# Performance work log

Measured on AMD Instinct MI355X. Metric: run time of the kernel, lower is better.

Reference implementation:

```python
import jax, jax.numpy as jnp
import numpy as np

B, S, DM, H = 2, 2048, 1024, 16
HD = DM // H


def setup_inputs() -> dict:
    key = jax.random.key(0)
    ks = jax.random.split(key, 12)
    xavier = lambda k: jax.random.uniform(k, (DM, DM), jnp.float32,
                                          -np.sqrt(6.0 / (DM + DM)), np.sqrt(6.0 / (DM + DM)))
    return {
        "q": jax.random.normal(ks[0], (B, S, DM), jnp.float32),
        "k": jax.random.normal(ks[1], (B, S, DM), jnp.float32),
        "v": jax.random.normal(ks[2], (B, S, DM), jnp.float32),
        "mask": jnp.ones((B, S, S), jnp.int32),
        "Wq": xavier(ks[3]), "bq": jnp.zeros((DM,), jnp.float32),
        "Wk": xavier(ks[4]), "bk": jnp.zeros((DM,), jnp.float32),
        "Wv": xavier(ks[5]), "bv": jnp.zeros((DM,), jnp.float32),
        "Wf": xavier(ks[6]), "bf": jnp.zeros((DM,), jnp.float32),
    }


def reference(q, k, v, mask, Wq, bq, Wk, bk, Wv, bv, Wf, bf):
    b, s, dm = q.shape
    # projections (torch Linear: x @ W.T + b)
    qh = (q @ Wq.T + bq).reshape(b, s, H, HD).transpose(0, 2, 1, 3)  # [B,H,S,HD]
    kh = (k @ Wk.T + bk).reshape(b, -1, H, HD).transpose(0, 2, 1, 3)
    vh = (v @ Wv.T + bv).reshape(b, -1, H, HD).transpose(0, 2, 1, 3)
    scores = jnp.einsum('bhqd,bhkd->bhqk', qh, kh) / np.sqrt(HD)    # [B,H,S,S]
    scores = jnp.where(mask[:, None, :, :] == 0, -jnp.inf, scores)
    attn = jax.nn.softmax(scores, axis=-1)
    out = jnp.einsum('bhqk,bhkd->bhqd', attn, vh)                   # [B,H,S,HD]
    out = out.transpose(0, 2, 1, 3).reshape(b, s, dm)
    return out @ Wf.T + bf, attn
```

## Files before the change

### kernel.cpp

```cpp
#include <hip/hip_runtime.h>
#include <stdint.h>


typedef _Float16 f16x8 __attribute__((ext_vector_type(8)));
typedef float f32x4 __attribute__((ext_vector_type(4)));
typedef unsigned long long ull;

static_assert(sizeof(f16x8) == 16, "f16x8 must be 16B");

#define MFMA16(a, b, c) __builtin_amdgcn_mfma_f32_16x16x32_f16((a), (b), (c), 0, 0, 0)

__device__ __forceinline__ unsigned short f2h_(float f) {
  _Float16 h = (_Float16)f;
  return __builtin_bit_cast(unsigned short, h);
}

__global__ __launch_bounds__(256) void cvt_kernel(
    const float* __restrict__ q, const float* __restrict__ k,
    const float* __restrict__ v, const float* __restrict__ wq,
    const float* __restrict__ wk, const float* __restrict__ wv,
    const float* __restrict__ wf, unsigned short* __restrict__ dst) {
  long e0 = ((long)blockIdx.x * 256 + threadIdx.x) * 8;
  const float* src; long off;
  if (e0 < 4194304L)       { src = q;  off = e0; }
  else if (e0 < 8388608L)  { src = k;  off = e0 - 4194304L; }
  else if (e0 < 12582912L) { src = v;  off = e0 - 8388608L; }
  else if (e0 < 13631488L) { src = wq; off = e0 - 12582912L; }
  else if (e0 < 14680064L) { src = wk; off = e0 - 13631488L; }
  else if (e0 < 15728640L) { src = wv; off = e0 - 14680064L; }
  else                     { src = wf; off = e0 - 15728640L; }
  float4 a = *(const float4*)(src + off);
  float4 b = *(const float4*)(src + off + 4);
  uint4 o;
  o.x = (unsigned)f2h_(a.x) | ((unsigned)f2h_(a.y) << 16);
  o.y = (unsigned)f2h_(a.z) | ((unsigned)f2h_(a.w) << 16);
  o.z = (unsigned)f2h_(b.x) | ((unsigned)f2h_(b.y) << 16);
  o.w = (unsigned)f2h_(b.z) | ((unsigned)f2h_(b.w) << 16);
  *(uint4*)(dst + e0) = o;
}

__global__ __launch_bounds__(256) void mask_pack(const int* __restrict__ mask,
                                                 ull* __restrict__ mb) {
  int wid = (int)((blockIdx.x * 256 + threadIdx.x) >> 6);
  int lane = threadIdx.x & 63;
  int nw = (int)((gridDim.x * 256) >> 6);
  for (int w = wid; w < 131072; w += nw) {
    int val = mask[(long)w * 64 + lane];
    ull bits = __ballot(val != 0);
    if (lane == 0) mb[w] = bits;
  }
}

__device__ __forceinline__ void gemm_body(
    const unsigned short* __restrict__ A, const unsigned short* __restrict__ Bm,
    const float* __restrict__ bias, unsigned short* __restrict__ outb,
    float* __restrict__ outf, int mode) {
  __shared__ unsigned short Al[128 * 64];
  __shared__ unsigned short Bl[128 * 64];
  const int tid = threadIdx.x, lane = tid & 63, wave = tid >> 6;
  const int lo = lane & 15, hi = lane >> 4;
  const int wi = wave >> 1, wj = wave & 1;
  const int ib = blockIdx.y << 7, jb = blockIdx.x << 7;
  const int cb0 = hi << 4;
  f32x4 acc[4][4] = {};
  for (int kt = 0; kt < 16; ++kt) {
    const int k0 = kt << 6;
    __syncthreads();
#pragma unroll
    for (int i = 0; i < 4; ++i) {
      int u = tid + (i << 8), r = u >> 3, c = u & 7;
      uint4 av = *(const uint4*)(A + (long)(ib + r) * 1024 + k0 + c * 8);
      uint4 bv = *(const uint4*)(Bm + (long)(jb + r) * 1024 + k0 + c * 8);
      *(uint4*)((char*)Al + r * 128 + ((c * 16) ^ ((r & 7) << 4))) = av;
      *(uint4*)((char*)Bl + r * 128 + ((c * 16) ^ ((r & 7) << 4))) = bv;
    }
    __syncthreads();
    f16x8 af[4][2], bfr[4][2];
#pragma unroll
    for (int it = 0; it < 4; ++it) {
      int r = (wi << 6) + (it << 4) + lo;
      af[it][0] = *(const f16x8*)((char*)Al + r * 128 + (cb0 ^ ((r & 7) << 4)));
      af[it][1] = *(const f16x8*)((char*)Al + r * 128 + ((64 + cb0) ^ ((r & 7) << 4)));
    }
#pragma unroll
    for (int jt = 0; jt < 4; ++jt) {
      int r = (wj << 6) + (jt << 4) + lo;
      bfr[jt][0] = *(const f16x8*)((char*)Bl + r * 128 + (cb0 ^ ((r & 7) << 4)));
      bfr[jt][1] = *(const f16x8*)((char*)Bl + r * 128 + ((64 + cb0) ^ ((r & 7) << 4)));
    }
#pragma unroll
    for (int it = 0; it < 4; ++it)
#pragma unroll
      for (int jt = 0; jt < 4; ++jt) {
        acc[it][jt] = MFMA16(af[it][0], bfr[jt][0], acc[it][jt]);
        acc[it][jt] = MFMA16(af[it][1], bfr[jt][1], acc[it][jt]);
      }
  }
#pragma unroll
  for (int it = 0; it < 4; ++it)
#pragma unroll
    for (int jt = 0; jt < 4; ++jt) {
      f32x4 vv = acc[it][jt];
      int i0 = ib + (wi << 6) + (it << 4) + (hi << 2);
      int j = jb + (wj << 6) + (jt << 4) + lo;
      float4 bb = *(const float4*)(bias + i0);
      vv[0] += bb.x; vv[1] += bb.y; vv[2] += bb.z; vv[3] += bb.w;
      if (mode == 2) {
        float4 st; st.x = vv[0]; st.y = vv[1]; st.z = vv[2]; st.w = vv[3];
        *(float4*)(outf + (long)j * 1024 + i0) = st;
      } else {
        int h = i0 >> 6, dd = i0 & 63, b2 = j >> 11, s2 = j & 2047;
        if (mode == 0) {
          ull pk = (ull)f2h_(vv[0]) | ((ull)f2h_(vv[1]) << 16) |
                   ((ull)f2h_(vv[2]) << 32) | ((ull)f2h_(vv[3]) << 48);
          *(ull*)(outb + ((long)((b2 * 16 + h) * 2048 + s2)) * 64 + dd) = pk;
        } else {
          unsigned short* p = outb + ((long)((b2 * 16 + h) * 64 + dd)) * 2048 + s2;
          p[0] = f2h_(vv[0]); p[2048] = f2h_(vv[1]);
          p[4096] = f2h_(vv[2]); p[6144] = f2h_(vv[3]);
        }
      }
    }
}

__global__ __launch_bounds__(256) void gemm_qkv(
    const unsigned short* __restrict__ xb, const float* __restrict__ bq,
    const float* __restrict__ bk, const float* __restrict__ bv,
    unsigned short* __restrict__ outbase) {
  const int z = blockIdx.z;
  const unsigned short* A = xb + 12582912 + (long)z * 1048576;
  const unsigned short* Bm = xb + (long)z * 4194304;
  const float* bias = (z == 0) ? bq : ((z == 1) ? bk : bv);
  unsigned short* outp = outbase + (long)z * 4194304;
  gemm_body(A, Bm, bias, outp, nullptr, (z == 2) ? 1 : 0);
}

__global__ __launch_bounds__(256) void gemm_f(
    const unsigned short* __restrict__ xb, const unsigned short* __restrict__ oh,
    const float* __restrict__ bias, float* __restrict__ outf) {
  gemm_body(xb + 15728640, oh, bias, nullptr, outf, 2);
}

__global__ __launch_bounds__(256) void attn_kernel(
    const unsigned short* __restrict__ qh, const unsigned short* __restrict__ kh,
    const unsigned short* __restrict__ vt, const ull* __restrict__ mb,
    float* __restrict__ attnp, unsigned short* __restrict__ oh) {
  __shared__ unsigned short Qs[64 * 64];
  __shared__ unsigned short Ks[128 * 64];
  __shared__ unsigned short Vs[64 * 128];
  __shared__ unsigned short Ps[64 * 128];
  const int tid = threadIdx.x, lane = tid & 63, wave = tid >> 6;
  const int lo = lane & 15, hi = lane >> 4;
  const int cb0 = hi << 4;
  int id = blockIdx.y * 32 + blockIdx.x;
  int wgid = (id & 7) * 128 + (id >> 3);
  const int bh = wgid >> 5, b_ = bh >> 4;
  const int q0 = (wgid & 31) << 6;
  const float cs = 0.18033688011112042f;

  {
    const unsigned short* qb = qh + ((long)bh * 2048 + q0) * 64;
#pragma unroll
    for (int i = 0; i < 2; ++i) {
      int u = tid + (i << 8), r = u >> 3, c = u & 7;
      uint4 d = *(const uint4*)(qb + r * 64 + c * 8);
      *(uint4*)((char*)Qs + r * 128 + ((c * 16) ^ ((r & 7) << 4))) = d;
    }
  }
  __syncthreads();
  const int rq = (wave << 4) + lo;
  const int qg = q0 + rq;
  const int swq = (rq & 7) << 4;
  f16x8 aq0 = *(const f16x8*)((char*)Qs + rq * 128 + (cb0 ^ swq));
  f16x8 aq1 = *(const f16x8*)((char*)Qs + rq * 128 + ((64 + cb0) ^ swq));
  const ull* mrow = mb + (long)(b_ * 2048 + qg) * 32;

  float ll = 0.f;
  f32x4 oacc[4] = {};

  for (int kt = 0; kt < 16; ++kt) {
    __syncthreads();
#pragma unroll
    for (int i = 0; i < 4; ++i) {
      int u = tid + (i << 8);
      { int r = u >> 3, c = u & 7;
        uint4 d = *(const uint4*)(kh + ((long)bh * 2048 + (kt << 7) + r) * 64 + c * 8);
        *(uint4*)((char*)Ks + r * 128 + ((c * 16) ^ ((r & 7) << 4))) = d; }
      { int r = u >> 4, c = u & 15;
        uint4 d = *(const uint4*)(vt + ((long)bh * 64 + r) * 2048 + (kt << 7) + c * 8);
        *(uint4*)((char*)Vs + r * 256 + ((c * 16) ^ ((r & 7) << 4))) = d; }
    }
    __syncthreads();
    f32x4 fa[8];
#pragma unroll
    for (int nt = 0; nt < 8; ++nt) {
      int rk = (nt << 4) + lo;
      int swk = (rk & 7) << 4;
      f16x8 k0 = *(const f16x8*)((char*)Ks + rk * 128 + (cb0 ^ swk));
      f16x8 k1 = *(const f16x8*)((char*)Ks + rk * 128 + ((64 + cb0) ^ swk));
      f32x4 z = {};
      z = MFMA16(k0, aq0, z);
      z = MFMA16(k1, aq1, z);
      fa[nt] = z;
    }
    ull mw0 = mrow[(kt << 1)], mw1 = mrow[(kt << 1) + 1];
    const bool fast = __all((mw0 & mw1) == ~0ull);
#pragma unroll
    for (int nt = 0; nt < 8; ++nt) {
      float e0 = __builtin_amdgcn_exp2f(fa[nt][0] * cs);
      float e1 = __builtin_amdgcn_exp2f(fa[nt][1] * cs);
      float e2 = __builtin_amdgcn_exp2f(fa[nt][2] * cs);
      float e3 = __builtin_amdgcn_exp2f(fa[nt][3] * cs);
      if (!fast) {
        int kb = (nt << 4) + (hi << 2);
        ull mws = (kb & 64) ? mw1 : mw0;
        int sh = kb & 63;
        if (!((mws >> sh) & 1ull)) e0 = 0.f;
        if (!((mws >> (sh + 1)) & 1ull)) e1 = 0.f;
        if (!((mws >> (sh + 2)) & 1ull)) e2 = 0.f;
        if (!((mws >> (sh + 3)) & 1ull)) e3 = 0.f;
      }
      ll += (e0 + e1) + (e2 + e3);
      ull pk = (ull)f2h_(e0) | ((ull)f2h_(e1) << 16) |
               ((ull)f2h_(e2) << 32) | ((ull)f2h_(e3) << 48);
      *(ull*)((char*)Ps + rq * 256 + (((nt << 5) + (hi << 3)) ^ swq)) = pk;
    }
    f16x8 ap[4];
#pragma unroll
    for (int ks = 0; ks < 4; ++ks)
      ap[ks] = *(const f16x8*)((char*)Ps + rq * 256 + (((ks << 6) + cb0) ^ swq));
#pragma unroll
    for (int nt = 0; nt < 4; ++nt) {
      int rv = (nt << 4) + lo;
      int swv = (rv & 7) << 4;
#pragma unroll
      for (int ks = 0; ks < 4; ++ks) {
        f16x8 bvv = *(const f16x8*)((char*)Vs + rv * 256 + (((ks << 6) + cb0) ^ swv));
        oacc[nt] = MFMA16(ap[ks], bvv, oacc[nt]);
      }
    }
  }
  ll += __shfl_xor(ll, 16);
  ll += __shfl_xor(ll, 32);
  const float rl = (ll > 0.f) ? (1.f / ll) : 0.f;

  float rlr[4];
#pragma unroll
  for (int r = 0; r < 4; ++r) rlr[r] = __shfl(rl, (hi << 2) + r, 16);
#pragma unroll
  for (int nt = 0; nt < 4; ++nt)
#pragma unroll
    for (int r = 0; r < 4; ++r) {
      int qe = q0 + (wave << 4) + (hi << 2) + r;
      oh[(long)(b_ * 2048 + qe) * 1024 + ((bh & 15) << 6) + (nt << 4) + lo] =
          f2h_(oacc[nt][r] * rlr[r]);
    }

  float* arow = attnp + ((long)bh * 2048 + qg) * 2048;
  for (int kt = 0; kt < 16; ++kt) {
    __syncthreads();
#pragma unroll
    for (int i = 0; i < 4; ++i) {
      int u = tid + (i << 8), r = u >> 3, c = u & 7;
      uint4 d = *(const uint4*)(kh + ((long)bh * 2048 + (kt << 7) + r) * 64 + c * 8);
      *(uint4*)((char*)Ks + r * 128 + ((c * 16) ^ ((r & 7) << 4))) = d;
    }
    __syncthreads();
    f32x4 fa[8];
#pragma unroll
    for (int nt = 0; nt < 8; ++nt) {
      int rk = (nt << 4) + lo;
      int swk = (rk & 7) << 4;
      f16x8 k0 = *(const f16x8*)((char*)Ks + rk * 128 + (cb0 ^ swk));
      f16x8 k1 = *(const f16x8*)((char*)Ks + rk * 128 + ((64 + cb0) ^ swk));
      f32x4 z = {};
      z = MFMA16(k0, aq0, z);
      z = MFMA16(k1, aq1, z);
      fa[nt] = z;
    }
    ull mw0 = mrow[(kt << 1)], mw1 = mrow[(kt << 1) + 1];
    const bool fast = __all((mw0 & mw1) == ~0ull);
#pragma unroll
    for (int nt = 0; nt < 8; ++nt) {
      float e0 = __builtin_amdgcn_exp2f(fa[nt][0] * cs) * rl;
      float e1 = __builtin_amdgcn_exp2f(fa[nt][1] * cs) * rl;
      float e2 = __builtin_amdgcn_exp2f(fa[nt][2] * cs) * rl;
      float e3 = __builtin_amdgcn_exp2f(fa[nt][3] * cs) * rl;
      if (!fast) {
        int kb = (nt << 4) + (hi << 2);
        ull mws = (kb & 64) ? mw1 : mw0;
        int sh = kb & 63;
        if (!((mws >> sh) & 1ull)) e0 = 0.f;
        if (!((mws >> (sh + 1)) & 1ull)) e1 = 0.f;
        if (!((mws >> (sh + 2)) & 1ull)) e2 = 0.f;
        if (!((mws >> (sh + 3)) & 1ull)) e3 = 0.f;
      }
      f32x4 st; st[0] = e0; st[1] = e1; st[2] = e2; st[3] = e3;
      __builtin_nontemporal_store(st, (f32x4*)(arow + (kt << 7) + (nt << 4) + (hi << 2)));
    }
  }
}

extern "C" void kernel_launch(void* const* d_in, const int* in_sizes, int n_in,
                              void* d_out, int out_size, void* d_ws, size_t ws_size,
                              hipStream_t stream) {
  const float* q = (const float*)d_in[0];
  const float* k = (const float*)d_in[1];
  const float* v = (const float*)d_in[2];
  const int* mask = (const int*)d_in[3];
  const float* Wq = (const float*)d_in[4];
  const float* bq = (const float*)d_in[5];
  const float* Wk = (const float*)d_in[6];
  const float* bk = (const float*)d_in[7];
  const float* Wv = (const float*)d_in[8];
  const float* bv = (const float*)d_in[9];
  const float* Wf = (const float*)d_in[10];
  const float* bf_ = (const float*)d_in[11];

  float* out = (float*)d_out;
  float* attn = out + 4194304;

  unsigned short* xb = (unsigned short*)d_ws;
  unsigned short* qhp = xb + 16777216;
  unsigned short* khp = qhp + 4194304;
  unsigned short* vtp = khp + 4194304;
  unsigned short* ohp = vtp + 4194304;
  ull* mb = (ull*)((char*)d_ws + 67108864);

  cvt_kernel<<<dim3(8192), dim3(256), 0, stream>>>(q, k, v, Wq, Wk, Wv, Wf, xb);
  mask_pack<<<dim3(512), dim3(256), 0, stream>>>(mask, mb);
  gemm_qkv<<<dim3(32, 8, 3), dim3(256), 0, stream>>>(xb, bq, bk, bv, qhp);
  attn_kernel<<<dim3(32, 32), dim3(256), 0, stream>>>(qhp, khp, vtp, mb, attn, ohp);
  gemm_f<<<dim3(32, 8), dim3(256), 0, stream>>>(xb, ohp, bf_, out);
}
```

Measured before the change: 315.1 us.

## Split attention into two kernels and load GEMM tiles directly into LDS

The GEMM tile loads now use global_load_lds so data goes straight into LDS, which drops the XOR swizzle and reads fragments from an unswizzled layout. The fused attention kernel is split in two. The first computes the output and the per-row reciprocal softmax sums, which go to workspace. The second recomputes the scores to write the normalized attention matrix and is launched after the final projection GEMM. Both attention kernels read K and V fragments straight from global memory instead of staging them in LDS, which removes the barriers. The trade-offs are possible LDS bank conflicts in the GEMM, less coalesced per-lane global fragment loads in attention, and an extra launch.

```diff
diff --git a/kernel.cpp b/kernel.cpp
--- a/kernel.cpp
+++ b/kernel.cpp
@@ -13,6 +13,12 @@
 __device__ __forceinline__ unsigned short f2h_(float f) {
   _Float16 h = (_Float16)f;
   return __builtin_bit_cast(unsigned short, h);
+}
+
+__device__ __forceinline__ void gload16(const void* g, void* l) {
+  __builtin_amdgcn_global_load_lds(
+      (const __attribute__((address_space(1))) unsigned int*)g,
+      (__attribute__((address_space(3))) unsigned int*)l, 16, 0, 0);
 }
 
 __global__ __launch_bounds__(256) void cvt_kernel(
@@ -62,31 +68,32 @@
   const int wi = wave >> 1, wj = wave & 1;
   const int ib = blockIdx.y << 7, jb = blockIdx.x << 7;
   const int cb0 = hi << 4;
+  const int sr = lane >> 3;
+  const int sc = (lane & 7) << 3;
   f32x4 acc[4][4] = {};
   for (int kt = 0; kt < 16; ++kt) {
     const int k0 = kt << 6;
     __syncthreads();
 #pragma unroll
     for (int i = 0; i < 4; ++i) {
-      int u = tid + (i << 8), r = u >> 3, c = u & 7;
-      uint4 av = *(const uint4*)(A + (long)(ib + r) * 1024 + k0 + c * 8);
-      uint4 bv = *(const uint4*)(Bm + (long)(jb + r) * 1024 + k0 + c * 8);
-      *(uint4*)((char*)Al + r * 128 + ((c * 16) ^ ((r & 7) << 4))) = av;
-      *(uint4*)((char*)Bl + r * 128 + ((c * 16) ^ ((r & 7) << 4))) = bv;
+      int ci = (i << 2) + wave;
+      int r = (ci << 3) + sr;
+      gload16(A + (long)(ib + r) * 1024 + k0 + sc, Al + (ci << 9));
+      gload16(Bm + (long)(jb + r) * 1024 + k0 + sc, Bl + (ci << 9));
     }
     __syncthreads();
     f16x8 af[4][2], bfr[4][2];
 #pragma unroll
     for (int it = 0; it < 4; ++it) {
       int r = (wi << 6) + (it << 4) + lo;
-      af[it][0] = *(const f16x8*)((char*)Al + r * 128 + (cb0 ^ ((r & 7) << 4)));
-      af[it][1] = *(const f16x8*)((char*)Al + r * 128 + ((64 + cb0) ^ ((r & 7) << 4)));
+      af[it][0] = *(const f16x8*)((const char*)Al + r * 128 + cb0);
+      af[it][1] = *(const f16x8*)((const char*)Al + r * 128 + 64 + cb0);
     }
 #pragma unroll
     for (int jt = 0; jt < 4; ++jt) {
       int r = (wj << 6) + (jt << 4) + lo;
-      bfr[jt][0] = *(const f16x8*)((char*)Bl + r * 128 + (cb0 ^ ((r & 7) << 4)));
-      bfr[jt][1] = *(const f16x8*)((char*)Bl + r * 128 + ((64 + cb0) ^ ((r & 7) << 4)));
+      bfr[jt][0] = *(const f16x8*)((const char*)Bl + r * 128 + cb0);
+      bfr[jt][1] = *(const f16x8*)((const char*)Bl + r * 128 + 64 + cb0);
     }
 #pragma unroll
     for (int it = 0; it < 4; ++it)
@@ -141,70 +148,47 @@
   gemm_body(xb + 15728640, oh, bias, nullptr, outf, 2);
 }
 
-__global__ __launch_bounds__(256) void attn_kernel(
+__global__ __launch_bounds__(256) void attn1_kernel(
     const unsigned short* __restrict__ qh, const unsigned short* __restrict__ kh,
     const unsigned short* __restrict__ vt, const ull* __restrict__ mb,
-    float* __restrict__ attnp, unsigned short* __restrict__ oh) {
-  __shared__ unsigned short Qs[64 * 64];
-  __shared__ unsigned short Ks[128 * 64];
-  __shared__ unsigned short Vs[64 * 128];
+    float* __restrict__ rlw, unsigned short* __restrict__ oh) {
   __shared__ unsigned short Ps[64 * 128];
   const int tid = threadIdx.x, lane = tid & 63, wave = tid >> 6;
   const int lo = lane & 15, hi = lane >> 4;
   const int cb0 = hi << 4;
-  int id = blockIdx.y * 32 + blockIdx.x;
+  int id = blockIdx.x;
   int wgid = (id & 7) * 128 + (id >> 3);
   const int bh = wgid >> 5, b_ = bh >> 4;
   const int q0 = (wgid & 31) << 6;
   const float cs = 0.18033688011112042f;
 
-  {
-    const unsigned short* qb = qh + ((long)bh * 2048 + q0) * 64;
-#pragma unroll
-    for (int i = 0; i < 2; ++i) {
-      int u = tid + (i << 8), r = u >> 3, c = u & 7;
-      uint4 d = *(const uint4*)(qb + r * 64 + c * 8);
-      *(uint4*)((char*)Qs + r * 128 + ((c * 16) ^ ((r & 7) << 4))) = d;
-    }
-  }
-  __syncthreads();
   const int rq = (wave << 4) + lo;
   const int qg = q0 + rq;
   const int swq = (rq & 7) << 4;
-  f16x8 aq0 = *(const f16x8*)((char*)Qs + rq * 128 + (cb0 ^ swq));
-  f16x8 aq1 = *(const f16x8*)((char*)Qs + rq * 128 + ((64 + cb0) ^ swq));
+  const unsigned short* qp = qh + ((long)bh * 2048 + qg) * 64;
+  f16x8 aq0 = *(const f16x8*)(qp + (hi << 3));
+  f16x8 aq1 = *(const f16x8*)(qp + 32 + (hi << 3));
   const ull* mrow = mb + (long)(b_ * 2048 + qg) * 32;
 
   float ll = 0.f;
   f32x4 oacc[4] = {};
 
   for (int kt = 0; kt < 16; ++kt) {
-    __syncthreads();
-#pragma unroll
-    for (int i = 0; i < 4; ++i) {
-      int u = tid + (i << 8);
-      { int r = u >> 3, c = u & 7;
-        uint4 d = *(const uint4*)(kh + ((long)bh * 2048 + (kt << 7) + r) * 64 + c * 8);
-        *(uint4*)((char*)Ks + r * 128 + ((c * 16) ^ ((r & 7) << 4))) = d; }
-      { int r = u >> 4, c = u & 15;
-        uint4 d = *(const uint4*)(vt + ((long)bh * 64 + r) * 2048 + (kt << 7) + c * 8);
-        *(uint4*)((char*)Vs + r * 256 + ((c * 16) ^ ((r & 7) << 4))) = d; }
-    }
-    __syncthreads();
+    const unsigned short* kbase = kh + ((long)bh * 2048 + (kt << 7)) * 64;
+    const unsigned short* vbase = vt + ((long)bh * 64) * 2048 + (kt << 7);
     f32x4 fa[8];
 #pragma unroll
     for (int nt = 0; nt < 8; ++nt) {
-      int rk = (nt << 4) + lo;
-      int swk = (rk & 7) << 4;
-      f16x8 k0 = *(const f16x8*)((char*)Ks + rk * 128 + (cb0 ^ swk));
-      f16x8 k1 = *(const f16x8*)((char*)Ks + rk * 128 + ((64 + cb0) ^ swk));
+      const unsigned short* kp = kbase + ((nt << 4) + lo) * 64;
+      f16x8 k0 = *(const f16x8*)(kp + (hi << 3));
+      f16x8 k1 = *(const f16x8*)(kp + 32 + (hi << 3));
       f32x4 z = {};
       z = MFMA16(k0, aq0, z);
       z = MFMA16(k1, aq1, z);
       fa[nt] = z;
     }
     ull mw0 = mrow[(kt << 1)], mw1 = mrow[(kt << 1) + 1];
-    const bool fast = __all((mw0 & mw1) == ~0ull);
+    const bool fast = __all((int)((mw0 & mw1) == ~0ull));
 #pragma unroll
     for (int nt = 0; nt < 8; ++nt) {
       float e0 = __builtin_amdgcn_exp2f(fa[nt][0] * cs);
@@ -231,11 +215,10 @@
       ap[ks] = *(const f16x8*)((char*)Ps + rq * 256 + (((ks << 6) + cb0) ^ swq));
 #pragma unroll
     for (int nt = 0; nt < 4; ++nt) {
-      int rv = (nt << 4) + lo;
-      int swv = (rv & 7) << 4;
+      const unsigned short* vp = vbase + ((long)((nt << 4) + lo)) * 2048;
 #pragma unroll
       for (int ks = 0; ks < 4; ++ks) {
-        f16x8 bvv = *(const f16x8*)((char*)Vs + rv * 256 + (((ks << 6) + cb0) ^ swv));
+        f16x8 bvv = *(const f16x8*)(vp + (ks << 5) + (hi << 3));
         oacc[nt] = MFMA16(ap[ks], bvv, oacc[nt]);
       }
     }
@@ -243,6 +226,7 @@
   ll += __shfl_xor(ll, 16);
   ll += __shfl_xor(ll, 32);
   const float rl = (ll > 0.f) ? (1.f / ll) : 0.f;
+  if (lane < 16) rlw[(long)bh * 2048 + q0 + (wave << 4) + lane] = rl;
 
   float rlr[4];
 #pragma unroll
@@ -255,31 +239,44 @@
       oh[(long)(b_ * 2048 + qe) * 1024 + ((bh & 15) << 6) + (nt << 4) + lo] =
           f2h_(oacc[nt][r] * rlr[r]);
     }
-
+}
+
+__global__ __launch_bounds__(256) void attn2_kernel(
+    const unsigned short* __restrict__ qh, const unsigned short* __restrict__ kh,
+    const ull* __restrict__ mb, const float* __restrict__ rlw,
+    float* __restrict__ attnp) {
+  const int tid = threadIdx.x, lane = tid & 63, wave = tid >> 6;
+  const int lo = lane & 15, hi = lane >> 4;
+  int id = blockIdx.x;
+  int wgid = (id & 7) * 128 + (id >> 3);
+  const int bh = wgid >> 5, b_ = bh >> 4;
+  const int q0 = (wgid & 31) << 6;
+  const float cs = 0.18033688011112042f;
+
+  const int rq = (wave << 4) + lo;
+  const int qg = q0 + rq;
+  const unsigned short* qp = qh + ((long)bh * 2048 + qg) * 64;
+  f16x8 aq0 = *(const f16x8*)(qp + (hi << 3));
+  f16x8 aq1 = *(const f16x8*)(qp + 32 + (hi << 3));
+  const float rl = rlw[(long)bh * 2048 + qg];
+  const ull* mrow = mb + (long)(b_ * 2048 + qg) * 32;
   float* arow = attnp + ((long)bh * 2048 + qg) * 2048;
+
   for (int kt = 0; kt < 16; ++kt) {
-    __syncthreads();
-#pragma unroll
-    for (int i = 0; i < 4; ++i) {
-      int u = tid + (i << 8), r = u >> 3, c = u & 7;
-      uint4 d = *(const uint4*)(kh + ((long)bh * 2048 + (kt << 7) + r) * 64 + c * 8);
-      *(uint4*)((char*)Ks + r * 128 + ((c * 16) ^ ((r & 7) << 4))) = d;
-    }
-    __syncthreads();
+    const unsigned short* kbase = kh + ((long)bh * 2048 + (kt << 7)) * 64;
     f32x4 fa[8];
 #pragma unroll
     for (int nt = 0; nt < 8; ++nt) {
-      int rk = (nt << 4) + lo;
-      int swk = (rk & 7) << 4;
-      f16x8 k0 = *(const f16x8*)((char*)Ks + rk * 128 + (cb0 ^ swk));
-      f16x8 k1 = *(const f16x8*)((char*)Ks + rk * 128 + ((64 + cb0) ^ swk));
+      const unsigned short* kp = kbase + ((nt << 4) + lo) * 64;
+      f16x8 k0 = *(const f16x8*)(kp + (hi << 3));
+      f16x8 k1 = *(const f16x8*)(kp + 32 + (hi << 3));
       f32x4 z = {};
       z = MFMA16(k0, aq0, z);
       z = MFMA16(k1, aq1, z);
       fa[nt] = z;
     }
     ull mw0 = mrow[(kt << 1)], mw1 = mrow[(kt << 1) + 1];
-    const bool fast = __all((mw0 & mw1) == ~0ull);
+    const bool fast = __all((int)((mw0 & mw1) == ~0ull));
 #pragma unroll
     for (int nt = 0; nt < 8; ++nt) {
       float e0 = __builtin_amdgcn_exp2f(fa[nt][0] * cs) * rl;
@@ -326,10 +323,12 @@
   unsigned short* vtp = khp + 4194304;
   unsigned short* ohp = vtp + 4194304;
   ull* mb = (ull*)((char*)d_ws + 67108864);
+  float* rlw = (float*)d_ws;
 
   cvt_kernel<<<dim3(8192), dim3(256), 0, stream>>>(q, k, v, Wq, Wk, Wv, Wf, xb);
   mask_pack<<<dim3(512), dim3(256), 0, stream>>>(mask, mb);
   gemm_qkv<<<dim3(32, 8, 3), dim3(256), 0, stream>>>(xb, bq, bk, bv, qhp);
-  attn_kernel<<<dim3(32, 32), dim3(256), 0, stream>>>(qhp, khp, vtp, mb, attn, ohp);
+  attn1_kernel<<<dim3(1024), dim3(256), 0, stream>>>(qhp, khp, vtp, mb, rlw, ohp);
   gemm_f<<<dim3(32, 8), dim3(256), 0, stream>>>(xb, ohp, bf_, out);
-}
+  attn2_kernel<<<dim3(1024), dim3(256), 0, stream>>>(qhp, khp, mb, rlw, attn);
+}
```

After: 558.1 us. 77.1% more time.

## Double attention query tile to 128 rows with 512-thread blocks

Applied to the files above, without the earlier changes.

The attention kernel now processes 128 query rows per workgroup with 8 waves instead of 64 rows with 4 waves. Each K/V tile loaded into shared memory is therefore reused by twice as many queries, halving the K/V global traffic and staging per query. Q is loaded directly from global into registers, skipping the shared-memory Q stage and one barrier. The cost is a larger shared-memory footprint (Ps doubles) and fewer, larger blocks, which may reduce occupancy. The hidden Ps write/read indexing must handle 8 waves for this to be correct.

```diff
diff --git a/kernel.cpp b/kernel.cpp
--- a/kernel.cpp
+++ b/kernel.cpp
@@ -141,39 +141,32 @@
   gemm_body(xb + 15728640, oh, bias, nullptr, outf, 2);
 }
 
-__global__ __launch_bounds__(256) void attn_kernel(
+__global__ __launch_bounds__(512, 4) void attn_kernel(
     const unsigned short* __restrict__ qh, const unsigned short* __restrict__ kh,
     const unsigned short* __restrict__ vt, const ull* __restrict__ mb,
     float* __restrict__ attnp, unsigned short* __restrict__ oh) {
-  __shared__ unsigned short Qs[64 * 64];
   __shared__ unsigned short Ks[128 * 64];
   __shared__ unsigned short Vs[64 * 128];
-  __shared__ unsigned short Ps[64 * 128];
+  __shared__ unsigned short Ps[128 * 128];
   const int tid = threadIdx.x, lane = tid & 63, wave = tid >> 6;
   const int lo = lane & 15, hi = lane >> 4;
   const int cb0 = hi << 4;
-  int id = blockIdx.y * 32 + blockIdx.x;
-  int wgid = (id & 7) * 128 + (id >> 3);
-  const int bh = wgid >> 5, b_ = bh >> 4;
-  const int q0 = (wgid & 31) << 6;
+  int id = blockIdx.x;
+  int wgid = (id & 7) * 64 + (id >> 3);
+  const int bh = wgid >> 4, b_ = bh >> 4;
+  const int q0 = (wgid & 15) << 7;
   const float cs = 0.18033688011112042f;
 
-  {
-    const unsigned short* qb = qh + ((long)bh * 2048 + q0) * 64;
-#pragma unroll
-    for (int i = 0; i < 2; ++i) {
-      int u = tid + (i << 8), r = u >> 3, c = u & 7;
-      uint4 d = *(const uint4*)(qb + r * 64 + c * 8);
-      *(uint4*)((char*)Qs + r * 128 + ((c * 16) ^ ((r & 7) << 4))) = d;
-    }
-  }
-  __syncthreads();
   const int rq = (wave << 4) + lo;
   const int qg = q0 + rq;
   const int swq = (rq & 7) << 4;
-  f16x8 aq0 = *(const f16x8*)((char*)Qs + rq * 128 + (cb0 ^ swq));
-  f16x8 aq1 = *(const f16x8*)((char*)Qs + rq * 128 + ((64 + cb0) ^ swq));
+  const unsigned short* qp = qh + ((long)bh * 2048 + qg) * 64;
+  f16x8 aq0 = *(const f16x8*)(qp + (hi << 3));
+  f16x8 aq1 = *(const f16x8*)(qp + 32 + (hi << 3));
   const ull* mrow = mb + (long)(b_ * 2048 + qg) * 32;
+
+  const unsigned short* kh_b = kh + (long)bh * 2048 * 64;
+  const unsigned short* vt_b = vt + (long)bh * 64 * 2048;
 
   float ll = 0.f;
   f32x4 oacc[4] = {};
@@ -181,13 +174,13 @@
   for (int kt = 0; kt < 16; ++kt) {
     __syncthreads();
 #pragma unroll
-    for (int i = 0; i < 4; ++i) {
-      int u = tid + (i << 8);
+    for (int i = 0; i < 2; ++i) {
+      int u = tid + (i << 9);
       { int r = u >> 3, c = u & 7;
-        uint4 d = *(const uint4*)(kh + ((long)bh * 2048 + (kt << 7) + r) * 64 + c * 8);
+        uint4 d = *(const uint4*)(kh_b + (long)(((kt) << 7) + r) * 64 + c * 8);
         *(uint4*)((char*)Ks + r * 128 + ((c * 16) ^ ((r & 7) << 4))) = d; }
       { int r = u >> 4, c = u & 15;
-        uint4 d = *(const uint4*)(vt + ((long)bh * 64 + r) * 2048 + (kt << 7) + c * 8);
+        uint4 d = *(const uint4*)(vt_b + (long)r * 2048 + (kt << 7) + c * 8);
         *(uint4*)((char*)Vs + r * 256 + ((c * 16) ^ ((r & 7) << 4))) = d; }
     }
     __syncthreads();
@@ -204,7 +197,7 @@
       fa[nt] = z;
     }
     ull mw0 = mrow[(kt << 1)], mw1 = mrow[(kt << 1) + 1];
-    const bool fast = __all((mw0 & mw1) == ~0ull);
+    const bool fast = __all((int)((mw0 & mw1) == ~0ull));
 #pragma unroll
     for (int nt = 0; nt < 8; ++nt) {
       float e0 = __builtin_amdgcn_exp2f(fa[nt][0] * cs);
@@ -260,9 +253,9 @@
   for (int kt = 0; kt < 16; ++kt) {
     __syncthreads();
 #pragma unroll
-    for (int i = 0; i < 4; ++i) {
-      int u = tid + (i << 8), r = u >> 3, c = u & 7;
-      uint4 d = *(const uint4*)(kh + ((long)bh * 2048 + (kt << 7) + r) * 64 + c * 8);
+    for (int i = 0; i < 2; ++i) {
+      int u = tid + (i << 9), r = u >> 3, c = u & 7;
+      uint4 d = *(const uint4*)(kh_b + (long)((kt << 7) + r) * 64 + c * 8);
       *(uint4*)((char*)Ks + r * 128 + ((c * 16) ^ ((r & 7) << 4))) = d;
     }
     __syncthreads();
@@ -279,7 +272,7 @@
       fa[nt] = z;
     }
     ull mw0 = mrow[(kt << 1)], mw1 = mrow[(kt << 1) + 1];
-    const bool fast = __all((mw0 & mw1) == ~0ull);
+    const bool fast = __all((int)((mw0 & mw1) == ~0ull));
 #pragma unroll
     for (int nt = 0; nt < 8; ++nt) {
       float e0 = __builtin_amdgcn_exp2f(fa[nt][0] * cs) * rl;
@@ -330,6 +323,6 @@
   cvt_kernel<<<dim3(8192), dim3(256), 0, stream>>>(q, k, v, Wq, Wk, Wv, Wf, xb);
   mask_pack<<<dim3(512), dim3(256), 0, stream>>>(mask, mb);
   gemm_qkv<<<dim3(32, 8, 3), dim3(256), 0, stream>>>(xb, bq, bk, bv, qhp);
-  attn_kernel<<<dim3(32, 32), dim3(256), 0, stream>>>(qhp, khp, vtp, mb, attn, ohp);
+  attn_kernel<<<dim3(512), dim3(512), 0, stream>>>(qhp, khp, vtp, mb, attn, ohp);
   gemm_f<<<dim3(32, 8), dim3(256), 0, stream>>>(xb, ohp, bf_, out);
 }
```

Measured after the change: 344.9 us. 1.09x slower.

## Split attention into output pass and separate normalized-probability writer kernel

Applied to the files above, without the earlier changes.

The fused attention kernel is split in two. The first kernel computes the softmax denominators and the attention output, then stores the reciprocal row sums to workspace. A second kernel, one block per (head, 128-key slice), keeps its K fragments in registers and loops over all queries to recompute the scores and stream out the normalized attention matrix without LDS or barriers. This trades an extra launch and a recomputation of QK^T for a write phase that is decoupled from the first pass and has no LDS staging.

```diff
diff --git a/kernel.cpp b/kernel.cpp
--- a/kernel.cpp
+++ b/kernel.cpp
@@ -141,10 +141,10 @@
   gemm_body(xb + 15728640, oh, bias, nullptr, outf, 2);
 }
 
-__global__ __launch_bounds__(256) void attn_kernel(
+__global__ __launch_bounds__(256) void attn1_kernel(
     const unsigned short* __restrict__ qh, const unsigned short* __restrict__ kh,
     const unsigned short* __restrict__ vt, const ull* __restrict__ mb,
-    float* __restrict__ attnp, unsigned short* __restrict__ oh) {
+    float* __restrict__ rlw, unsigned short* __restrict__ oh) {
   __shared__ unsigned short Qs[64 * 64];
   __shared__ unsigned short Ks[128 * 64];
   __shared__ unsigned short Vs[64 * 128];
@@ -152,7 +152,7 @@
   const int tid = threadIdx.x, lane = tid & 63, wave = tid >> 6;
   const int lo = lane & 15, hi = lane >> 4;
   const int cb0 = hi << 4;
-  int id = blockIdx.y * 32 + blockIdx.x;
+  int id = blockIdx.x;
   int wgid = (id & 7) * 128 + (id >> 3);
   const int bh = wgid >> 5, b_ = bh >> 4;
   const int q0 = (wgid & 31) << 6;
@@ -204,7 +204,7 @@
       fa[nt] = z;
     }
     ull mw0 = mrow[(kt << 1)], mw1 = mrow[(kt << 1) + 1];
-    const bool fast = __all((mw0 & mw1) == ~0ull);
+    const bool fast = __all((int)((mw0 & mw1) == ~0ull));
 #pragma unroll
     for (int nt = 0; nt < 8; ++nt) {
       float e0 = __builtin_amdgcn_exp2f(fa[nt][0] * cs);
@@ -243,6 +243,7 @@
   ll += __shfl_xor(ll, 16);
   ll += __shfl_xor(ll, 32);
   const float rl = (ll > 0.f) ? (1.f / ll) : 0.f;
+  if (lane < 16) rlw[(long)bh * 2048 + q0 + (wave << 4) + lane] = rl;
 
   float rlr[4];
 #pragma unroll
@@ -255,31 +256,47 @@
       oh[(long)(b_ * 2048 + qe) * 1024 + ((bh & 15) << 6) + (nt << 4) + lo] =
           f2h_(oacc[nt][r] * rlr[r]);
     }
-
-  float* arow = attnp + ((long)bh * 2048 + qg) * 2048;
-  for (int kt = 0; kt < 16; ++kt) {
-    __syncthreads();
-#pragma unroll
-    for (int i = 0; i < 4; ++i) {
-      int u = tid + (i << 8), r = u >> 3, c = u & 7;
-      uint4 d = *(const uint4*)(kh + ((long)bh * 2048 + (kt << 7) + r) * 64 + c * 8);
-      *(uint4*)((char*)Ks + r * 128 + ((c * 16) ^ ((r & 7) << 4))) = d;
-    }
-    __syncthreads();
+}
+
+__global__ __launch_bounds__(256) void attn2_kernel(
+    const unsigned short* __restrict__ qh, const unsigned short* __restrict__ kh,
+    const ull* __restrict__ mb, const float* __restrict__ rlw,
+    float* __restrict__ attnp) {
+  const int tid = threadIdx.x, lane = tid & 63, wave = tid >> 6;
+  const int lo = lane & 15, hi = lane >> 4;
+  int id = blockIdx.x;
+  int wgid = (id & 7) * 64 + (id >> 3);
+  const int bh = wgid >> 4, b_ = bh >> 4;
+  const int ksl = wgid & 15;
+  const float cs = 0.18033688011112042f;
+
+  const unsigned short* kbase = kh + ((long)bh * 2048 + (ksl << 7)) * 64;
+  f16x8 kf[8][2];
+#pragma unroll
+  for (int nt = 0; nt < 8; ++nt) {
+    const unsigned short* kp = kbase + ((nt << 4) + lo) * 64;
+    kf[nt][0] = *(const f16x8*)(kp + (hi << 3));
+    kf[nt][1] = *(const f16x8*)(kp + 32 + (hi << 3));
+  }
+
+  for (int it = 0; it < 32; ++it) {
+    const int qg = (it << 6) + (wave << 4) + lo;
+    const unsigned short* qp = qh + ((long)bh * 2048 + qg) * 64;
+    f16x8 aq0 = *(const f16x8*)(qp + (hi << 3));
+    f16x8 aq1 = *(const f16x8*)(qp + 32 + (hi << 3));
+    const float rl = rlw[(long)bh * 2048 + qg];
+    const ull* mrow = mb + (long)(b_ * 2048 + qg) * 32;
+    ull mw0 = mrow[ksl << 1], mw1 = mrow[(ksl << 1) + 1];
+    const bool fast = __all((int)((mw0 & mw1) == ~0ull));
     f32x4 fa[8];
 #pragma unroll
     for (int nt = 0; nt < 8; ++nt) {
-      int rk = (nt << 4) + lo;
-      int swk = (rk & 7) << 4;
-      f16x8 k0 = *(const f16x8*)((char*)Ks + rk * 128 + (cb0 ^ swk));
-      f16x8 k1 = *(const f16x8*)((char*)Ks + rk * 128 + ((64 + cb0) ^ swk));
       f32x4 z = {};
-      z = MFMA16(k0, aq0, z);
-      z = MFMA16(k1, aq1, z);
+      z = MFMA16(kf[nt][0], aq0, z);
+      z = MFMA16(kf[nt][1], aq1, z);
       fa[nt] = z;
     }
-    ull mw0 = mrow[(kt << 1)], mw1 = mrow[(kt << 1) + 1];
-    const bool fast = __all((mw0 & mw1) == ~0ull);
+    float* arow = attnp + ((long)bh * 2048 + qg) * 2048 + (ksl << 7);
 #pragma unroll
     for (int nt = 0; nt < 8; ++nt) {
       float e0 = __builtin_amdgcn_exp2f(fa[nt][0] * cs) * rl;
@@ -296,7 +313,7 @@
         if (!((mws >> (sh + 3)) & 1ull)) e3 = 0.f;
       }
       f32x4 st; st[0] = e0; st[1] = e1; st[2] = e2; st[3] = e3;
-      __builtin_nontemporal_store(st, (f32x4*)(arow + (kt << 7) + (nt << 4) + (hi << 2)));
+      __builtin_nontemporal_store(st, (f32x4*)(arow + (nt << 4) + (hi << 2)));
     }
   }
 }
@@ -326,10 +343,12 @@
   unsigned short* vtp = khp + 4194304;
   unsigned short* ohp = vtp + 4194304;
   ull* mb = (ull*)((char*)d_ws + 67108864);
+  float* rlw = (float*)(xb + 8388608);
 
   cvt_kernel<<<dim3(8192), dim3(256), 0, stream>>>(q, k, v, Wq, Wk, Wv, Wf, xb);
   mask_pack<<<dim3(512), dim3(256), 0, stream>>>(mask, mb);
   gemm_qkv<<<dim3(32, 8, 3), dim3(256), 0, stream>>>(xb, bq, bk, bv, qhp);
-  attn_kernel<<<dim3(32, 32), dim3(256), 0, stream>>>(qhp, khp, vtp, mb, attn, ohp);
+  attn1_kernel<<<dim3(1024), dim3(256), 0, stream>>>(qhp, khp, vtp, mb, rlw, ohp);
+  attn2_kernel<<<dim3(512), dim3(256), 0, stream>>>(qhp, khp, mb, rlw, attn);
   gemm_f<<<dim3(32, 8), dim3(256), 0, stream>>>(xb, ohp, bf_, out);
 }
```

Measured after the change: 352.0 us. 11.7% more time.
